# Performance work log

Hardware: AMD Instinct MI355X
Metric: run time of the kernel (lower is better)

## Reference

```python
import jax, jax.numpy as jnp
import numpy as np

N, D, IN, OUT, K = 50000, 16, 256, 128, 4  # nodes, sampled degree, input_size, output_size, heads
LEAKY_SLOPE = 0.01  # torch F.leaky_relu default


def setup_inputs() -> dict:
    key = jax.random.key(0)
    k1, k2, k3, k4 = jax.random.split(key, 4)
    X = jax.random.normal(k1, (N, IN), dtype=jnp.float32)
    W = jax.random.normal(k2, (K, OUT, IN), dtype=jnp.float32) * 0.05
    a = jax.random.normal(k3, (K, 2 * OUT), dtype=jnp.float32) * 0.05
    neighbor_idx = jax.random.randint(k4, (N, D), 0, N)  # fixed-degree neighbor sample
    return {"X": X, "W": W, "a": a, "neighbor_idx": neighbor_idx}


def reference(X, W, a, neighbor_idx):
    # X: [N, IN]; W: [K, OUT, IN]; a: [K, 2*OUT]; neighbor_idx: [N, D]
    out_dim = W.shape[1]
    # Per-head linear map of every node once: Wh[k, n] = W[k] @ X[n]
    Wh = jnp.einsum('koi,ni->kno', W, X)                       # [K, N, OUT]
    # a splits: first OUT weights multiply mapped neighbour, second OUT multiply mapped self
    a_nb, a_self = a[:, :out_dim], a[:, out_dim:]
    e_nb = jnp.einsum('kno,ko->kn', Wh, a_nb)                  # [K, N] score contribution as a neighbour
    e_self = jnp.einsum('kno,ko->kn', Wh, a_self)              # [K, N] score contribution as center node
    # Edge logits: e[k, i, d] = leaky_relu(a_nb.Wh[j] + a_self.Wh[i]), j = neighbor_idx[i, d]
    e = jax.nn.leaky_relu(e_nb[:, neighbor_idx] + e_self[:, :, None], LEAKY_SLOPE)  # [K, N, D]
    alpha = jax.nn.softmax(e, axis=-1)                         # softmax over each node's neighbour set
    Wh_nb = jnp.take(Wh, neighbor_idx, axis=1)                 # [K, N, D, OUT] gathered neighbour features
    h = jnp.einsum('knd,kndo->kno', alpha, Wh_nb)              # [K, N, OUT] attention-weighted aggregate
    # Concatenate heads along feature dim, matching per-node head-concat in the torch loop
    return jnp.transpose(h, (1, 0, 2)).reshape(X.shape[0], -1)  # [N, K*OUT]
```

## Files before the change

### kernel.cpp

```cpp
#include <hip/hip_runtime.h>

#define N_NODES 50000
#define D_NB 16
#define IN_DIM 256
#define OUT_DIM 128
#define K_HEADS 4
#define SLOPE 0.01f

typedef __attribute__((ext_vector_type(8))) short short8;
typedef __attribute__((ext_vector_type(4))) float f32x4;

static __device__ __forceinline__ unsigned short f2bf(float f) {
    unsigned u = __float_as_uint(f);
    unsigned r = u + 0x7fffu + ((u >> 16) & 1u);
    return (unsigned short)(r >> 16);
}
static __device__ __forceinline__ float bf2f(unsigned short b) {
    return __uint_as_float(((unsigned)b) << 16);
}

__global__ void wb_kernel(const float* __restrict__ W, unsigned short* __restrict__ Wb) {
    int id = blockIdx.x * blockDim.x + threadIdx.x;
    if (id < K_HEADS * OUT_DIM * IN_DIM) Wb[id] = f2bf(W[id]);
}

__global__ __launch_bounds__(256) void gemm_kernel(
    const float* __restrict__ X, const unsigned short* __restrict__ Wb,
    const float* __restrict__ a,
    unsigned short* __restrict__ Whb, float* __restrict__ e_nb, float* __restrict__ e_self)
{
    __shared__ unsigned short Wlds[64 * IN_DIM];

    const int t = threadIdx.x;
    const int lane = t & 63;
    const int w = t >> 6;
    const int lrow = lane & 15;
    const int lk = lane >> 4;
    const int m0 = blockIdx.x * 64 + w * 16;

    const int arow = m0 + lrow;
    const bool avalid = arow < N_NODES;
    const float* Xr = X + (size_t)arow * IN_DIM + lk * 8;
    short8 af[8];
    #pragma unroll
    for (int kk = 0; kk < 8; ++kk) {
        short8 s;
        if (avalid) {
            float4 x0 = *(const float4*)(Xr + kk * 32);
            float4 x1 = *(const float4*)(Xr + kk * 32 + 4);
            s[0] = (short)f2bf(x0.x); s[1] = (short)f2bf(x0.y);
            s[2] = (short)f2bf(x0.z); s[3] = (short)f2bf(x0.w);
            s[4] = (short)f2bf(x1.x); s[5] = (short)f2bf(x1.y);
            s[6] = (short)f2bf(x1.z); s[7] = (short)f2bf(x1.w);
        } else {
            s = short8{0, 0, 0, 0, 0, 0, 0, 0};
        }
        af[kk] = s;
    }

    for (int k = 0; k < K_HEADS; ++k) {
        float pnb = 0.f, psf = 0.f;
        #pragma unroll
        for (int h = 0; h < 2; ++h) {
            if (k | h) __syncthreads();
            {
                const unsigned short* WbH = Wb + ((size_t)k * OUT_DIM + h * 64) * IN_DIM;
                #pragma unroll
                for (int i = 0; i < 8; ++i) {
                    const int c = i * 256 + w * 64 + lane;
                    const int r = c >> 5;
                    const int p = c & 31;
                    const int cu = p ^ (r & 7);
                    const unsigned short* gsrc = WbH + r * IN_DIM + cu * 8;
                    unsigned short* ldst = &Wlds[(size_t)(i * 256 + w * 64) * 8];
                    __builtin_amdgcn_global_load_lds(
                        (const __attribute__((address_space(1))) void*)gsrc,
                        (__attribute__((address_space(3))) void*)ldst, 16, 0, 0);
                }
            }
            __syncthreads();

            f32x4 acc[4] = {};
            #pragma unroll
            for (int kk = 0; kk < 8; ++kk) {
                #pragma unroll
                for (int nt = 0; nt < 4; ++nt) {
                    const int row = nt * 16 + lrow;
                    const int pos = (kk * 4 + lk) ^ (row & 7);
                    const short8 bf = *(const short8*)(&Wlds[row * IN_DIM + pos * 8]);
                    acc[nt] = __builtin_amdgcn_mfma_f32_16x16x32_bf16(bf, af[kk], acc[nt], 0, 0, 0);
                }
            }

            #pragma unroll
            for (int nt = 0; nt < 4; ++nt) {
                const float4 anb = *(const float4*)(a + k * 2 * OUT_DIM + h * 64 + nt * 16 + lk * 4);
                const float4 asf = *(const float4*)(a + k * 2 * OUT_DIM + OUT_DIM + h * 64 + nt * 16 + lk * 4);
                pnb += acc[nt][0] * anb.x + acc[nt][1] * anb.y
                     + acc[nt][2] * anb.z + acc[nt][3] * anb.w;
                psf += acc[nt][0] * asf.x + acc[nt][1] * asf.y
                     + acc[nt][2] * asf.z + acc[nt][3] * asf.w;
            }
            if (avalid) {
                unsigned short* dst = Whb + (size_t)arow * (K_HEADS * OUT_DIM) + k * OUT_DIM + h * 64;
                #pragma unroll
                for (int nt = 0; nt < 4; ++nt) {
                    uint2 pk;
                    pk.x = (unsigned)f2bf(acc[nt][0]) | ((unsigned)f2bf(acc[nt][1]) << 16);
                    pk.y = (unsigned)f2bf(acc[nt][2]) | ((unsigned)f2bf(acc[nt][3]) << 16);
                    *(uint2*)(dst + nt * 16 + lk * 4) = pk;
                }
            }
        }
        pnb += __shfl_xor(pnb, 16); pnb += __shfl_xor(pnb, 32);
        psf += __shfl_xor(psf, 16); psf += __shfl_xor(psf, 32);
        if (avalid && lane < 16) {
            e_nb[(size_t)arow * K_HEADS + k] = pnb;
            e_self[(size_t)arow * K_HEADS + k] = psf;
        }
    }
}

__global__ __launch_bounds__(256) void attn_kernel(
    const int* __restrict__ nidx, const unsigned short* __restrict__ Whb,
    const float* __restrict__ e_nb, const float* __restrict__ e_self,
    float* __restrict__ out)
{
    const int w = threadIdx.x >> 6;
    const int lane = threadIdx.x & 63;
    const int n0 = (blockIdx.x * 4 + w) * 2;
    const int n1 = n0 + 1;
    const int kl = lane >> 4;
    const int dl = lane & 15;

    const int nbr0 = nidx[(size_t)n0 * D_NB + dl];
    const int nbr1 = nidx[(size_t)n1 * D_NB + dl];
    const float x0 = e_nb[(size_t)nbr0 * K_HEADS + kl] + e_self[(size_t)n0 * K_HEADS + kl];
    const float x1 = e_nb[(size_t)nbr1 * K_HEADS + kl] + e_self[(size_t)n1 * K_HEADS + kl];
    const float v0 = x0 > 0.f ? x0 : SLOPE * x0;
    const float v1 = x1 > 0.f ? x1 : SLOPE * x1;
    float m0 = v0, m1 = v1;
    #pragma unroll
    for (int s = 8; s >= 1; s >>= 1) {
        m0 = fmaxf(m0, __shfl_xor(m0, s, 16));
        m1 = fmaxf(m1, __shfl_xor(m1, s, 16));
    }
    const float p0 = __expf(v0 - m0);
    const float p1 = __expf(v1 - m1);
    float s0 = p0, s1 = p1;
    #pragma unroll
    for (int s = 8; s >= 1; s >>= 1) {
        s0 += __shfl_xor(s0, s, 16);
        s1 += __shfl_xor(s1, s, 16);
    }
    const float alpha0 = p0 / s0;
    const float alpha1 = p1 / s1;

    float acc0[8] = {}, acc1[8] = {};
    #pragma unroll
    for (int d = 0; d < D_NB; ++d) {
        const float ad0 = __shfl(alpha0, kl * 16 + d);
        const int nd0 = __shfl(nbr0, d);
        const float ad1 = __shfl(alpha1, kl * 16 + d);
        const int nd1 = __shfl(nbr1, d);
        const short8 va = *(const short8*)(Whb + (size_t)nd0 * (K_HEADS * OUT_DIM) + lane * 8);
        const short8 vb = *(const short8*)(Whb + (size_t)nd1 * (K_HEADS * OUT_DIM) + lane * 8);
        #pragma unroll
        for (int j = 0; j < 8; ++j) {
            acc0[j] += ad0 * bf2f((unsigned short)va[j]);
            acc1[j] += ad1 * bf2f((unsigned short)vb[j]);
        }
    }
    float* op0 = out + (size_t)n0 * (K_HEADS * OUT_DIM) + lane * 8;
    *(float4*)op0       = float4{acc0[0], acc0[1], acc0[2], acc0[3]};
    *(float4*)(op0 + 4) = float4{acc0[4], acc0[5], acc0[6], acc0[7]};
    float* op1 = out + (size_t)n1 * (K_HEADS * OUT_DIM) + lane * 8;
    *(float4*)op1       = float4{acc1[0], acc1[1], acc1[2], acc1[3]};
    *(float4*)(op1 + 4) = float4{acc1[4], acc1[5], acc1[6], acc1[7]};
}

extern "C" void kernel_launch(void* const* d_in, const int* in_sizes, int n_in,
                              void* d_out, int out_size, void* d_ws, size_t ws_size,
                              hipStream_t stream) {
    const float* X = (const float*)d_in[0];
    const float* W = (const float*)d_in[1];
    const float* a = (const float*)d_in[2];
    const int* nidx = (const int*)d_in[3];
    float* out = (float*)d_out;

    char* p = (char*)d_ws;
    unsigned short* Wb = (unsigned short*)p;      p += (size_t)K_HEADS * OUT_DIM * IN_DIM * 2;
    unsigned short* Whb = (unsigned short*)p;     p += (size_t)N_NODES * K_HEADS * OUT_DIM * 2;
    float* enb = (float*)p;                       p += (size_t)N_NODES * K_HEADS * 4;
    float* eself = (float*)p;

    hipLaunchKernelGGL(wb_kernel,
        dim3((K_HEADS * OUT_DIM * IN_DIM + 255) / 256), dim3(256), 0, stream, W, Wb);

    hipLaunchKernelGGL(gemm_kernel,
        dim3((N_NODES + 63) / 64), dim3(256), 0, stream, X, Wb, a, Whb, enb, eself);

    hipLaunchKernelGGL(attn_kernel,
        dim3(N_NODES / 8), dim3(256), 0, stream, nidx, Whb, enb, eself, out);
}
```

Before: 185.3 us.

## Slice Wh into column panels and pin each panel pair to one XCD for L2-local gathers

The GEMM now writes Wh as 16 slice-major panels of 32 columns (N×32 each) and double-buffers the weight slice in LDS, prefetching the next slice while the current one is computed. The attention kernel launches a fixed grid in which blockIdx&7 selects a pair of panels, so each XCD gathers only its own ~6.4MB of Wh. This keeps the random neighbour gathers inside that XCD's L2 instead of pulling the full 51MB table across every cache. In exchange the gathers become 4-byte-per-lane loads, softmax logits are recomputed per slice pair, and the speedup relies on blocks being assigned to XCDs round-robin by block index.

```diff
diff --git a/kernel.cpp b/kernel.cpp
--- a/kernel.cpp
+++ b/kernel.cpp
@@ -6,6 +6,8 @@
 #define OUT_DIM 128
 #define K_HEADS 4
 #define SLOPE 0.01f
+#define NSLICE 16
+#define SLICE_COLS 32
 
 typedef __attribute__((ext_vector_type(8))) short short8;
 typedef __attribute__((ext_vector_type(4))) float f32x4;
@@ -27,9 +29,9 @@
 __global__ __launch_bounds__(256) void gemm_kernel(
     const float* __restrict__ X, const unsigned short* __restrict__ Wb,
     const float* __restrict__ a,
-    unsigned short* __restrict__ Whb, float* __restrict__ e_nb, float* __restrict__ e_self)
+    unsigned short* __restrict__ Whb2, float* __restrict__ e_nb, float* __restrict__ e_self)
 {
-    __shared__ unsigned short Wlds[64 * IN_DIM];
+    __shared__ unsigned short Wlds[2][SLICE_COLS * IN_DIM];
 
     const int t = threadIdx.x;
     const int lane = t & 63;
@@ -40,6 +42,7 @@
 
     const int arow = m0 + lrow;
     const bool avalid = arow < N_NODES;
+
     const float* Xr = X + (size_t)arow * IN_DIM + lk * 8;
     short8 af[8];
     #pragma unroll
@@ -58,125 +61,120 @@
         af[kk] = s;
     }
 
-    for (int k = 0; k < K_HEADS; ++k) {
-        float pnb = 0.f, psf = 0.f;
-        #pragma unroll
-        for (int h = 0; h < 2; ++h) {
-            if (k | h) __syncthreads();
-            {
-                const unsigned short* WbH = Wb + ((size_t)k * OUT_DIM + h * 64) * IN_DIM;
-                #pragma unroll
-                for (int i = 0; i < 8; ++i) {
-                    const int c = i * 256 + w * 64 + lane;
-                    const int r = c >> 5;
-                    const int p = c & 31;
-                    const int cu = p ^ (r & 7);
-                    const unsigned short* gsrc = WbH + r * IN_DIM + cu * 8;
-                    unsigned short* ldst = &Wlds[(size_t)(i * 256 + w * 64) * 8];
-                    __builtin_amdgcn_global_load_lds(
-                        (const __attribute__((address_space(1))) void*)gsrc,
-                        (__attribute__((address_space(3))) void*)ldst, 16, 0, 0);
-                }
+    auto STAGE = [&](int st, int buf) {
+        const unsigned short* WbS = Wb + (size_t)st * SLICE_COLS * IN_DIM;
+        #pragma unroll
+        for (int i = 0; i < 4; ++i) {
+            const int c = i * 256 + t;
+            const int r = c >> 5;
+            const int p = c & 31;
+            const int cu = p ^ (r & 7);
+            const unsigned short* gsrc = WbS + r * IN_DIM + cu * 8;
+            unsigned short* ldst = &Wlds[buf][c * 8];
+            __builtin_amdgcn_global_load_lds(
+                (const __attribute__((address_space(1))) void*)gsrc,
+                (__attribute__((address_space(3))) void*)ldst, 16, 0, 0);
+        }
+    };
+
+    float pnb = 0.f, psf = 0.f;
+    STAGE(0, 0);
+    __syncthreads();
+
+    for (int st = 0; st < NSLICE; ++st) {
+        const int buf = st & 1;
+        if (st + 1 < NSLICE) STAGE(st + 1, buf ^ 1);
+
+        f32x4 acc[2] = {};
+        #pragma unroll
+        for (int kk = 0; kk < 8; ++kk) {
+            #pragma unroll
+            for (int nt = 0; nt < 2; ++nt) {
+                const int row = nt * 16 + lrow;
+                const int pos = (kk * 4 + lk) ^ (row & 7);
+                const short8 bf = *(const short8*)(&Wlds[buf][row * IN_DIM + pos * 8]);
+                acc[nt] = __builtin_amdgcn_mfma_f32_16x16x32_bf16(bf, af[kk], acc[nt], 0, 0, 0);
             }
-            __syncthreads();
-
-            f32x4 acc[4] = {};
-            #pragma unroll
-            for (int kk = 0; kk < 8; ++kk) {
-                #pragma unroll
-                for (int nt = 0; nt < 4; ++nt) {
-                    const int row = nt * 16 + lrow;
-                    const int pos = (kk * 4 + lk) ^ (row & 7);
-                    const short8 bf = *(const short8*)(&Wlds[row * IN_DIM + pos * 8]);
-                    acc[nt] = __builtin_amdgcn_mfma_f32_16x16x32_bf16(bf, af[kk], acc[nt], 0, 0, 0);
-                }
+        }
+
+        const int k = st >> 2, cb = st & 3;
+        #pragma unroll
+        for (int nt = 0; nt < 2; ++nt) {
+            const float4 anb = *(const float4*)(a + k * 2 * OUT_DIM + cb * 32 + nt * 16 + lk * 4);
+            const float4 asf = *(const float4*)(a + k * 2 * OUT_DIM + OUT_DIM + cb * 32 + nt * 16 + lk * 4);
+            pnb += acc[nt][0] * anb.x + acc[nt][1] * anb.y
+                 + acc[nt][2] * anb.z + acc[nt][3] * anb.w;
+            psf += acc[nt][0] * asf.x + acc[nt][1] * asf.y
+                 + acc[nt][2] * asf.z + acc[nt][3] * asf.w;
+            if (avalid) {
+                uint2 pk;
+                pk.x = (unsigned)f2bf(acc[nt][0]) | ((unsigned)f2bf(acc[nt][1]) << 16);
+                pk.y = (unsigned)f2bf(acc[nt][2]) | ((unsigned)f2bf(acc[nt][3]) << 16);
+                *(uint2*)(Whb2 + ((size_t)st * N_NODES + arow) * SLICE_COLS + nt * 16 + lk * 4) = pk;
             }
-
-            #pragma unroll
-            for (int nt = 0; nt < 4; ++nt) {
-                const float4 anb = *(const float4*)(a + k * 2 * OUT_DIM + h * 64 + nt * 16 + lk * 4);
-                const float4 asf = *(const float4*)(a + k * 2 * OUT_DIM + OUT_DIM + h * 64 + nt * 16 + lk * 4);
-                pnb += acc[nt][0] * anb.x + acc[nt][1] * anb.y
-                     + acc[nt][2] * anb.z + acc[nt][3] * anb.w;
-                psf += acc[nt][0] * asf.x + acc[nt][1] * asf.y
-                     + acc[nt][2] * asf.z + acc[nt][3] * asf.w;
+        }
+        if ((st & 3) == 3) {
+            pnb += __shfl_xor(pnb, 16); pnb += __shfl_xor(pnb, 32);
+            psf += __shfl_xor(psf, 16); psf += __shfl_xor(psf, 32);
+            if (avalid && lane < 16) {
+                e_nb[(size_t)arow * K_HEADS + k] = pnb;
+                e_self[(size_t)arow * K_HEADS + k] = psf;
             }
-            if (avalid) {
-                unsigned short* dst = Whb + (size_t)arow * (K_HEADS * OUT_DIM) + k * OUT_DIM + h * 64;
-                #pragma unroll
-                for (int nt = 0; nt < 4; ++nt) {
-                    uint2 pk;
-                    pk.x = (unsigned)f2bf(acc[nt][0]) | ((unsigned)f2bf(acc[nt][1]) << 16);
-                    pk.y = (unsigned)f2bf(acc[nt][2]) | ((unsigned)f2bf(acc[nt][3]) << 16);
-                    *(uint2*)(dst + nt * 16 + lk * 4) = pk;
-                }
-            }
-        }
-        pnb += __shfl_xor(pnb, 16); pnb += __shfl_xor(pnb, 32);
-        psf += __shfl_xor(psf, 16); psf += __shfl_xor(psf, 32);
-        if (avalid && lane < 16) {
-            e_nb[(size_t)arow * K_HEADS + k] = pnb;
-            e_self[(size_t)arow * K_HEADS + k] = psf;
-        }
+            pnb = 0.f; psf = 0.f;
+        }
+        __syncthreads();
     }
 }
 
 __global__ __launch_bounds__(256) void attn_kernel(
-    const int* __restrict__ nidx, const unsigned short* __restrict__ Whb,
+    const int* __restrict__ nidx, const unsigned short* __restrict__ Whb2,
     const float* __restrict__ e_nb, const float* __restrict__ e_self,
     float* __restrict__ out)
 {
+    const int xcd = blockIdx.x & 7;
+    const int slot = blockIdx.x >> 3;
     const int w = threadIdx.x >> 6;
     const int lane = threadIdx.x & 63;
-    const int n0 = (blockIdx.x * 4 + w) * 2;
-    const int n1 = n0 + 1;
-    const int kl = lane >> 4;
-    const int dl = lane & 15;
-
-    const int nbr0 = nidx[(size_t)n0 * D_NB + dl];
-    const int nbr1 = nidx[(size_t)n1 * D_NB + dl];
-    const float x0 = e_nb[(size_t)nbr0 * K_HEADS + kl] + e_self[(size_t)n0 * K_HEADS + kl];
-    const float x1 = e_nb[(size_t)nbr1 * K_HEADS + kl] + e_self[(size_t)n1 * K_HEADS + kl];
-    const float v0 = x0 > 0.f ? x0 : SLOPE * x0;
-    const float v1 = x1 > 0.f ? x1 : SLOPE * x1;
-    float m0 = v0, m1 = v1;
-    #pragma unroll
-    for (int s = 8; s >= 1; s >>= 1) {
-        m0 = fmaxf(m0, __shfl_xor(m0, s, 16));
-        m1 = fmaxf(m1, __shfl_xor(m1, s, 16));
+    const int nl = lane >> 4;
+    const int d = lane & 15;
+    const int s0 = xcd * 2;
+    const int k = s0 >> 2;
+    const int cb0 = s0 & 3;
+    const unsigned short* S0 = Whb2 + (size_t)s0 * N_NODES * SLICE_COLS;
+    const unsigned short* S1 = S0 + (size_t)N_NODES * SLICE_COLS;
+
+    for (int i = slot; i < N_NODES / 16; i += 128) {
+        const int n = i * 16 + w * 4 + nl;
+
+        const int nbr = nidx[(size_t)n * D_NB + d];
+        const float x = e_nb[(size_t)nbr * K_HEADS + k] + e_self[(size_t)n * K_HEADS + k];
+        const float v = x > 0.f ? x : SLOPE * x;
+        float m = v;
+        #pragma unroll
+        for (int s = 8; s >= 1; s >>= 1) m = fmaxf(m, __shfl_xor(m, s, 16));
+        const float p = __expf(v - m);
+        float sum = p;
+        #pragma unroll
+        for (int s = 8; s >= 1; s >>= 1) sum += __shfl_xor(sum, s, 16);
+        const float alpha = p / sum;
+
+        float a0 = 0.f, a1 = 0.f, a2 = 0.f, a3 = 0.f;
+        #pragma unroll
+        for (int dd = 0; dd < D_NB; ++dd) {
+            const int src = (lane & 48) | dd;
+            const float ad = __shfl(alpha, src);
+            const int nd = __shfl(nbr, src);
+            const unsigned u0 = *(const unsigned*)(S0 + (size_t)nd * SLICE_COLS + d * 2);
+            const unsigned u1 = *(const unsigned*)(S1 + (size_t)nd * SLICE_COLS + d * 2);
+            a0 += ad * bf2f((unsigned short)(u0 & 0xffffu));
+            a1 += ad * bf2f((unsigned short)(u0 >> 16));
+            a2 += ad * bf2f((unsigned short)(u1 & 0xffffu));
+            a3 += ad * bf2f((unsigned short)(u1 >> 16));
+        }
+        float* op = out + (size_t)n * (K_HEADS * OUT_DIM) + k * OUT_DIM + cb0 * SLICE_COLS + d * 2;
+        *(float2*)op        = float2{a0, a1};
+        *(float2*)(op + 32) = float2{a2, a3};
     }
-    const float p0 = __expf(v0 - m0);
-    const float p1 = __expf(v1 - m1);
-    float s0 = p0, s1 = p1;
-    #pragma unroll
-    for (int s = 8; s >= 1; s >>= 1) {
-        s0 += __shfl_xor(s0, s, 16);
-        s1 += __shfl_xor(s1, s, 16);
-    }
-    const float alpha0 = p0 / s0;
-    const float alpha1 = p1 / s1;
-
-    float acc0[8] = {}, acc1[8] = {};
-    #pragma unroll
-    for (int d = 0; d < D_NB; ++d) {
-        const float ad0 = __shfl(alpha0, kl * 16 + d);
-        const int nd0 = __shfl(nbr0, d);
-        const float ad1 = __shfl(alpha1, kl * 16 + d);
-        const int nd1 = __shfl(nbr1, d);
-        const short8 va = *(const short8*)(Whb + (size_t)nd0 * (K_HEADS * OUT_DIM) + lane * 8);
-        const short8 vb = *(const short8*)(Whb + (size_t)nd1 * (K_HEADS * OUT_DIM) + lane * 8);
-        #pragma unroll
-        for (int j = 0; j < 8; ++j) {
-            acc0[j] += ad0 * bf2f((unsigned short)va[j]);
-            acc1[j] += ad1 * bf2f((unsigned short)vb[j]);
-        }
-    }
-    float* op0 = out + (size_t)n0 * (K_HEADS * OUT_DIM) + lane * 8;
-    *(float4*)op0       = float4{acc0[0], acc0[1], acc0[2], acc0[3]};
-    *(float4*)(op0 + 4) = float4{acc0[4], acc0[5], acc0[6], acc0[7]};
-    float* op1 = out + (size_t)n1 * (K_HEADS * OUT_DIM) + lane * 8;
-    *(float4*)op1       = float4{acc1[0], acc1[1], acc1[2], acc1[3]};
-    *(float4*)(op1 + 4) = float4{acc1[4], acc1[5], acc1[6], acc1[7]};
 }
 
 extern "C" void kernel_launch(void* const* d_in, const int* in_sizes, int n_in,
@@ -190,7 +188,7 @@
 
     char* p = (char*)d_ws;
     unsigned short* Wb = (unsigned short*)p;      p += (size_t)K_HEADS * OUT_DIM * IN_DIM * 2;
-    unsigned short* Whb = (unsigned short*)p;     p += (size_t)N_NODES * K_HEADS * OUT_DIM * 2;
+    unsigned short* Whb2 = (unsigned short*)p;    p += (size_t)NSLICE * N_NODES * SLICE_COLS * 2;
     float* enb = (float*)p;                       p += (size_t)N_NODES * K_HEADS * 4;
     float* eself = (float*)p;
 
@@ -198,8 +196,8 @@
         dim3((K_HEADS * OUT_DIM * IN_DIM + 255) / 256), dim3(256), 0, stream, W, Wb);
 
     hipLaunchKernelGGL(gemm_kernel,
-        dim3((N_NODES + 63) / 64), dim3(256), 0, stream, X, Wb, a, Whb, enb, eself);
+        dim3((N_NODES + 63) / 64), dim3(256), 0, stream, X, Wb, a, Whb2, enb, eself);
 
     hipLaunchKernelGGL(attn_kernel,
-        dim3(N_NODES / 8), dim3(256), 0, stream, nidx, Whb, enb, eself, out);
-}
+        dim3(8 * 128), dim3(256), 0, stream, nidx, Whb2, enb, eself, out);
+}
```

New measurement: 192.5 us. 1.04x slower.
